# Kernel optimization log

Hardware: AMD Instinct MI355X
Metric: run time of the kernel (lower is better)

The kernel has to match this reference:

```python
import jax, jax.numpy as jnp
import numpy as np

NUM_HEADS = 8
EPS_OT = 0.05    # self.eps
BETA_T = 1.0     # self.beta_t
N_ITERS = 100    # Sinkhorn max_iter (reference runs all iterations; torch breaks early on convergence)


def setup_inputs() -> dict:
    key = jax.random.key(0)
    ks = jax.random.split(key, 10)
    B, N1, N2 = 16, 256, 576
    dim_t, dim_v, dim_out = 512, 512, 512
    s = 0.02  # conv1d k=1 init scale (stand-in for torch default init)
    f32 = jnp.float32
    return {
        "F_t": jax.random.normal(ks[0], (B, N1, dim_t), f32),
        "F_s": jax.random.normal(ks[1], (B, N2, dim_v), f32),
        # Conv1d(kernel_size=1) weights, squeezed to [out, in]; biases default-on in nn.Conv1d
        "Wq": jax.random.normal(ks[2], (dim_out, dim_t), f32) * s,
        "bq": jnp.zeros((dim_out,), f32),
        "Wk": jax.random.normal(ks[3], (dim_out, dim_v), f32) * s,
        "bk": jnp.zeros((dim_out,), f32),
        "Wv": jax.random.normal(ks[4], (dim_out, dim_v), f32) * s,
        "bv": jnp.zeros((dim_out,), f32),
        "Wp": jax.random.normal(ks[5], (dim_out, dim_out), f32) * s,
        "bp": jnp.zeros((dim_out,), f32),
    }


def sinkhorn_log_exp_sum(C, log_mu, log_nu, eps):
    # C: [BH, N1, N2]; fixed-length log-domain Sinkhorn.
    BH, N1, N2 = C.shape
    u0 = jnp.zeros((BH, N1), C.dtype)
    v0 = jnp.zeros((BH, N2), C.dtype)

    def body(carry, _):
        u, v = carry
        # single K per iteration; both u and v updates use the OLD (u, v), matching torch code
        K = (-C + u[:, :, None] + v[:, None, :]) / eps
        u_new = eps * (log_mu - jax.scipy.special.logsumexp(K, axis=2)) + u
        v_new = eps * (log_nu - jax.scipy.special.logsumexp(K, axis=1)) + v
        return (u_new, v_new), None

    (u, v), _ = jax.lax.scan(jax.checkpoint(body), (u0, v0), None, length=N_ITERS)
    return jnp.exp((-C + u[:, :, None] + v[:, None, :]) / eps)


def _l2norm(x, eps=1e-12):
    return x / jnp.maximum(jnp.linalg.norm(x, axis=-1, keepdims=True), eps)


def reference(F_t, F_s, Wq, bq, Wk, bk, Wv, bv, Wp, bp):
    B, N1, _ = F_t.shape
    N2 = F_s.shape[1]
    H = NUM_HEADS
    dim_out = Wq.shape[0]
    hd = dim_out // H

    # Conv1d(kernel=1) == pointwise linear over channel dim
    q = (F_t @ Wq.T + bq).reshape(B, N1, H, hd)
    k = (F_s @ Wk.T + bk).reshape(B, N2, H, hd)
    v = (F_s @ Wv.T + bv).reshape(B, N2, H, hd)

    q = _l2norm(q)
    k = _l2norm(k)

    sim = jnp.einsum('bnkc,bmkc->bknm', q, k) * BETA_T  # [B,H,N1,N2]
    wdist = (1.0 - sim).reshape(B * H, N1, N2)
    sim_f = sim.reshape(B * H, N1, N2)

    log_mu = jnp.log(jnp.asarray(1.0 / N1 + 1e-8, sim.dtype))
    log_nu = jnp.log(jnp.asarray(1.0 / N2 + 1e-8, sim.dtype))
    T = sinkhorn_log_exp_sum(wdist, log_mu, log_nu, EPS_OT)

    score_map = (N1 * N2 * sim_f * T).reshape(B, H, N1, N2)  # attn_drop = identity (p=0)
    F_t_a = jnp.einsum('bknm,bmkc->bnkc', score_map, v).reshape(B, N1, dim_out)
    F_t_a = F_t_a @ Wp.T + bp
    # torch: F_t_a / F_t_a.norm(dim=-1, keepdim=True)  (plain division, no eps clamp)
    F_t_a = F_t_a / jnp.linalg.norm(F_t_a, axis=-1, keepdims=True)
    return F_t_a  # proj_drop = identity (p=0)
```

## Files before the change

### kernel.cpp

```cpp
#include <hip/hip_runtime.h>
#include <math.h>

#define EPS_OT 0.05f
#define INV_EPS 20.0f

typedef unsigned short ushort_t;
typedef __attribute__((ext_vector_type(8))) short short8;
typedef __attribute__((ext_vector_type(4))) float f32x4;
union Pk { uint4 u; short8 s; };

__device__ __forceinline__ unsigned int f2bf(float f) {
  unsigned int u = __float_as_uint(f);
  return (u + 0x7FFFu + ((u >> 16) & 1u)) >> 16;
}
__device__ __forceinline__ float bf2f(unsigned int u) { return __uint_as_float(u << 16); }

__global__ __launch_bounds__(256) void pack_k(const float* __restrict__ F_t,
                                              const float* __restrict__ F_s,
                                              const float* __restrict__ Wq,
                                              const float* __restrict__ Wk,
                                              const float* __restrict__ Wv,
                                              const float* __restrict__ Wp,
                                              ushort_t* __restrict__ Fth, ushort_t* __restrict__ Ftl,
                                              ushort_t* __restrict__ Fsh, ushort_t* __restrict__ Fsl,
                                              ushort_t* __restrict__ Wqh, ushort_t* __restrict__ Wql,
                                              ushort_t* __restrict__ Wkh, ushort_t* __restrict__ Wkl,
                                              ushort_t* __restrict__ Wvh, ushort_t* __restrict__ Wvl,
                                              ushort_t* __restrict__ Wph) {
  const int blk = blockIdx.x;
  const float* src; ushort_t* dh; ushort_t* dl; size_t off;
  if (blk < 2048)      { src = F_t; dh = Fth; dl = Ftl; off = (size_t)blk * 1024; }
  else if (blk < 6656) { src = F_s; dh = Fsh; dl = Fsl; off = (size_t)(blk - 2048) * 1024; }
  else if (blk < 6912) { src = Wq;  dh = Wqh; dl = Wql; off = (size_t)(blk - 6656) * 1024; }
  else if (blk < 7168) { src = Wk;  dh = Wkh; dl = Wkl; off = (size_t)(blk - 6912) * 1024; }
  else if (blk < 7424) { src = Wv;  dh = Wvh; dl = Wvl; off = (size_t)(blk - 7168) * 1024; }
  else                 { src = Wp;  dh = Wph; dl = nullptr; off = (size_t)(blk - 7424) * 1024; }
  const size_t i = off + (size_t)threadIdx.x * 4;
  float4 f = *(const float4*)(src + i);
  unsigned int h0 = f2bf(f.x), h1 = f2bf(f.y), h2 = f2bf(f.z), h3 = f2bf(f.w);
  uint2 hh; hh.x = h0 | (h1 << 16); hh.y = h2 | (h3 << 16);
  *(uint2*)(dh + i) = hh;
  if (dl) {
    uint2 ll;
    ll.x = f2bf(f.x - bf2f(h0)) | (f2bf(f.y - bf2f(h1)) << 16);
    ll.y = f2bf(f.z - bf2f(h2)) | (f2bf(f.w - bf2f(h3)) << 16);
    *(uint2*)(dl + i) = ll;
  }
}

#define GEMM_HL_BODY()                                                                      \
  f32x4 acc[4] = {};                                                                        \
  for (int k0 = 0; k0 < 512; k0 += 64) {                                                    \
    uint4 a0 = *(const uint4*)(Xp_h + k0), a1 = *(const uint4*)(Xp_h + k0 + 8);             \
    uint4 b0 = *(const uint4*)(Xp_l + k0), b1 = *(const uint4*)(Xp_l + k0 + 8);             \
    uint4 c0 = *(const uint4*)(Wp_h + k0), c1 = *(const uint4*)(Wp_h + k0 + 8);             \
    uint4 d0 = *(const uint4*)(Wp_l + k0), d1 = *(const uint4*)(Wp_l + k0 + 8);             \
    __syncthreads();                                                                        \
    *(uint4*)&Xh[r][cg * 16] = a0; *(uint4*)&Xh[r][cg * 16 + 8] = a1;                       \
    *(uint4*)&Xl[r][cg * 16] = b0; *(uint4*)&Xl[r][cg * 16 + 8] = b1;                       \
    *(uint4*)&Wh[r][cg * 16] = c0; *(uint4*)&Wh[r][cg * 16 + 8] = c1;                       \
    *(uint4*)&Wl[r][cg * 16] = d0; *(uint4*)&Wl[r][cg * 16 + 8] = d1;                       \
    __syncthreads();                                                                        \
    _Pragma("unroll") for (int kst = 0; kst < 2; ++kst) {                                   \
      short8 ah = *(const short8*)&Xh[16 * w + li][kst * 32 + 8 * lg];                      \
      short8 al = *(const short8*)&Xl[16 * w + li][kst * 32 + 8 * lg];                      \
      _Pragma("unroll") for (int nt = 0; nt < 4; ++nt) {                                    \
        short8 bh = *(const short8*)&Wh[nt * 16 + li][kst * 32 + 8 * lg];                   \
        short8 bl = *(const short8*)&Wl[nt * 16 + li][kst * 32 + 8 * lg];                   \
        acc[nt] = __builtin_amdgcn_mfma_f32_16x16x32_bf16(ah, bh, acc[nt], 0, 0, 0);        \
        acc[nt] = __builtin_amdgcn_mfma_f32_16x16x32_bf16(ah, bl, acc[nt], 0, 0, 0);        \
        acc[nt] = __builtin_amdgcn_mfma_f32_16x16x32_bf16(al, bh, acc[nt], 0, 0, 0);        \
      }                                                                                     \
    }                                                                                       \
  }

#define GEMM_PL_BODY()                                                                      \
  f32x4 acc[4] = {};                                                                        \
  for (int k0 = 0; k0 < 512; k0 += 64) {                                                    \
    uint4 a0 = *(const uint4*)(Xp_h + k0), a1 = *(const uint4*)(Xp_h + k0 + 8);             \
    uint4 c0 = *(const uint4*)(Wp_h + k0), c1 = *(const uint4*)(Wp_h + k0 + 8);             \
    __syncthreads();                                                                        \
    *(uint4*)&Xh[r][cg * 16] = a0; *(uint4*)&Xh[r][cg * 16 + 8] = a1;                       \
    *(uint4*)&Wh[r][cg * 16] = c0; *(uint4*)&Wh[r][cg * 16 + 8] = c1;                       \
    __syncthreads();                                                                        \
    _Pragma("unroll") for (int kst = 0; kst < 2; ++kst) {                                   \
      short8 ah = *(const short8*)&Xh[16 * w + li][kst * 32 + 8 * lg];                      \
      _Pragma("unroll") for (int nt = 0; nt < 4; ++nt) {                                    \
        short8 bh = *(const short8*)&Wh[nt * 16 + li][kst * 32 + 8 * lg];                   \
        acc[nt] = __builtin_amdgcn_mfma_f32_16x16x32_bf16(ah, bh, acc[nt], 0, 0, 0);        \
      }                                                                                     \
    }                                                                                       \
  }

__global__ __launch_bounds__(256) void gemmnorm2_k(const ushort_t* __restrict__ Xg_h,
                                                   const ushort_t* __restrict__ Xg_l,
                                                   const ushort_t* __restrict__ Wg_h,
                                                   const ushort_t* __restrict__ Wg_l,
                                                   const float* __restrict__ bias,
                                                   ushort_t* __restrict__ oh,
                                                   ushort_t* __restrict__ ol, int Nn) {
  __shared__ ushort_t Xh[64][72], Xl[64][72], Wh[64][72], Wl[64][72];
  const int tid = threadIdx.x;
  const int w = tid >> 6, l = tid & 63, li = l & 15, lg = l >> 4;
  const int r = tid >> 2, cg = tid & 3;
  const int m0 = blockIdx.x << 6;
  const int h = blockIdx.y, n0 = h << 6;
  const ushort_t* Xp_h = Xg_h + (size_t)(m0 + r) * 512 + cg * 16;
  const ushort_t* Xp_l = Xg_l + (size_t)(m0 + r) * 512 + cg * 16;
  const ushort_t* Wp_h = Wg_h + (size_t)(n0 + r) * 512 + cg * 16;
  const ushort_t* Wp_l = Wg_l + (size_t)(n0 + r) * 512 + cg * 16;
  GEMM_HL_BODY()
  float v[4][4];
  float ss[4] = {0.f, 0.f, 0.f, 0.f};
#pragma unroll
  for (int nt = 0; nt < 4; ++nt) {
    float bb = bias[n0 + nt * 16 + li];
#pragma unroll
    for (int reg = 0; reg < 4; ++reg) {
      float y = acc[nt][reg] + bb;
      v[nt][reg] = y;
      ss[reg] = fmaf(y, y, ss[reg]);
    }
  }
#pragma unroll
  for (int off = 1; off < 16; off <<= 1)
#pragma unroll
    for (int reg = 0; reg < 4; ++reg) ss[reg] += __shfl_xor(ss[reg], off, 64);
  const int b = m0 / Nn;
  const int nbase = m0 - b * Nn;
  const size_t base = ((size_t)(b * 8 + h) * Nn + nbase + 16 * w + 4 * lg) * 64;
#pragma unroll
  for (int reg = 0; reg < 4; ++reg) {
    float inv = 1.0f / fmaxf(sqrtf(ss[reg]), 1e-12f);
#pragma unroll
    for (int nt = 0; nt < 4; ++nt) {
      float y = v[nt][reg] * inv;
      unsigned int hi = f2bf(y);
      size_t idx = base + (size_t)reg * 64 + nt * 16 + li;
      oh[idx] = (ushort_t)hi;
      ol[idx] = (ushort_t)f2bf(y - bf2f(hi));
    }
  }
}

__global__ __launch_bounds__(256) void gemmtrans2_k(const ushort_t* __restrict__ Xg_h,
                                                    const ushort_t* __restrict__ Wg_h,
                                                    const float* __restrict__ bias,
                                                    ushort_t* __restrict__ vt) {
  __shared__ ushort_t Xh[64][72], Wh[64][72];
  __shared__ ushort_t Vs[64 * 73];
  const int tid = threadIdx.x;
  const int w = tid >> 6, l = tid & 63, li = l & 15, lg = l >> 4;
  const int r = tid >> 2, cg = tid & 3;
  const int m0 = blockIdx.x << 6;
  const int h = blockIdx.y, n0 = h << 6;
  const ushort_t* Xp_h = Xg_h + (size_t)(m0 + r) * 512 + cg * 16;
  const ushort_t* Wp_h = Wg_h + (size_t)(n0 + r) * 512 + cg * 16;
  GEMM_PL_BODY()
#pragma unroll
  for (int nt = 0; nt < 4; ++nt) {
    float bb = bias[n0 + nt * 16 + li];
#pragma unroll
    for (int reg = 0; reg < 4; ++reg)
      Vs[(16 * w + 4 * lg + reg) * 73 + nt * 16 + li] = (ushort_t)f2bf(acc[nt][reg] + bb);
  }
  __syncthreads();
  const int a9 = m0 >> 6;
  const int b = a9 / 9;
  const int nbase = m0 - b * 576;
  const int s = b * 8 + h;
  const int c = tid >> 2, q4 = tid & 3;
  ushort_t tmp[16];
#pragma unroll
  for (int jj = 0; jj < 16; ++jj) tmp[jj] = Vs[(q4 * 16 + jj) * 73 + c];
  ushort_t* op = vt + ((size_t)s * 64 + c) * 576 + nbase + q4 * 16;
  *(uint4*)op = *(uint4*)&tmp[0];
  *(uint4*)(op + 8) = *(uint4*)&tmp[8];
}

__global__ __launch_bounds__(256) void gemmplain_k(const ushort_t* __restrict__ Xg_h,
                                                   const ushort_t* __restrict__ Wg_h,
                                                   const float* __restrict__ bias,
                                                   float* __restrict__ Y) {
  __shared__ ushort_t Xh[64][72], Wh[64][72];
  const int tid = threadIdx.x;
  const int w = tid >> 6, l = tid & 63, li = l & 15, lg = l >> 4;
  const int r = tid >> 2, cg = tid & 3;
  const int m0 = blockIdx.x << 6, n0 = blockIdx.y << 6;
  const ushort_t* Xp_h = Xg_h + (size_t)(m0 + r) * 512 + cg * 16;
  const ushort_t* Wp_h = Wg_h + (size_t)(n0 + r) * 512 + cg * 16;
  GEMM_PL_BODY()
#pragma unroll
  for (int nt = 0; nt < 4; ++nt) {
    float bb = bias[n0 + nt * 16 + li];
#pragma unroll
    for (int reg = 0; reg < 4; ++reg)
      Y[(size_t)(m0 + 16 * w + 4 * lg + reg) * 512 + n0 + nt * 16 + li] = acc[nt][reg] + bb;
  }
}

__global__ __launch_bounds__(256) void simE2_k(const ushort_t* __restrict__ qh,
                                               const ushort_t* __restrict__ ql,
                                               const ushort_t* __restrict__ kh,
                                               const ushort_t* __restrict__ kl,
                                               ushort_t* __restrict__ E) {
  const int s = blockIdx.x, i0 = blockIdx.y << 6, j0 = blockIdx.z << 6;
  const int tid = threadIdx.x;
  const int w = tid >> 6, l = tid & 63, li = l & 15, lg = l >> 4;
  const size_t qoff = ((size_t)s * 256 + i0 + 16 * w + li) * 64 + 8 * lg;
  short8 aH0 = *(const short8*)(qh + qoff), aH1 = *(const short8*)(qh + qoff + 32);
  short8 aL0 = *(const short8*)(ql + qoff), aL1 = *(const short8*)(ql + qoff + 32);
  f32x4 acc[4] = {};
#pragma unroll
  for (int nt = 0; nt < 4; ++nt) {
    const size_t koff = ((size_t)s * 576 + j0 + nt * 16 + li) * 64 + 8 * lg;
    short8 bH0 = *(const short8*)(kh + koff), bH1 = *(const short8*)(kh + koff + 32);
    short8 bL0 = *(const short8*)(kl + koff), bL1 = *(const short8*)(kl + koff + 32);
    acc[nt] = __builtin_amdgcn_mfma_f32_16x16x32_bf16(aH0, bH0, acc[nt], 0, 0, 0);
    acc[nt] = __builtin_amdgcn_mfma_f32_16x16x32_bf16(aH1, bH1, acc[nt], 0, 0, 0);
    acc[nt] = __builtin_amdgcn_mfma_f32_16x16x32_bf16(aH0, bL0, acc[nt], 0, 0, 0);
    acc[nt] = __builtin_amdgcn_mfma_f32_16x16x32_bf16(aH1, bL1, acc[nt], 0, 0, 0);
    acc[nt] = __builtin_amdgcn_mfma_f32_16x16x32_bf16(aL0, bH0, acc[nt], 0, 0, 0);
    acc[nt] = __builtin_amdgcn_mfma_f32_16x16x32_bf16(aL1, bH1, acc[nt], 0, 0, 0);
  }
  ushort_t* Ep = E + (size_t)s * 147456;
#pragma unroll
  for (int nt = 0; nt < 4; ++nt)
#pragma unroll
    for (int reg = 0; reg < 4; ++reg) {
      float e = __expf((acc[nt][reg] - 1.0f) * INV_EPS);
      Ep[(size_t)(i0 + 16 * w + 4 * lg + reg) * 576 + j0 + nt * 16 + li] = (ushort_t)f2bf(e);
    }
}

#define SK_SMEM 147456

__global__ __launch_bounds__(1024, 1) void sinkhorn8_k(const ushort_t* __restrict__ E,
                                                       float* __restrict__ gA,
                                                       float* __restrict__ gB,
                                                       unsigned long long* __restrict__ gpart,
                                                       float C_mu, float C_nu) {
  extern __shared__ char smem[];
  const int g = blockIdx.x, s = g >> 1, rh = g & 1, pg = g ^ 1;
  const int tid = threadIdx.x, w = tid >> 6, l = tid & 63, li = l & 15, lg = l >> 4;
  unsigned long long* myP = gpart + (size_t)g * 1152;
  const unsigned long long* prP = gpart + (size_t)pg * 1152;

  ushort_t* Elds = (ushort_t*)smem;
  {
    const uint4* Eg = (const uint4*)(E + (size_t)s * 147456 + (size_t)rh * 73728);
    uint4* El4 = (uint4*)Elds;
    for (int idx = tid; idx < 9216; idx += 1024) El4[idx] = Eg[idx];
  }
  __syncthreads();

  short8 afr[9];
#pragma unroll
  for (int rt = 0; rt < 8; ++rt)
    afr[rt] = *(const short8*)(Elds + (rt * 16 + li) * 576 + w * 32 + 8 * lg);
  const int rtx = w & 7, ktx = 16 + (w >> 3);
  afr[8] = *(const short8*)(Elds + (rtx * 16 + li) * 576 + ktx * 32 + 8 * lg);
  const int ktB = w >> 2, ntb = (w & 3) * 9;
  short8 bfr[9];
#pragma unroll
  for (int p9 = 0; p9 < 9; ++p9) {
    const ushort_t* p = Elds + (ktB * 32 + 8 * lg) * 576 + (ntb + p9) * 16 + li;
    Pk pk;
    pk.u.x = (unsigned int)p[0]    | ((unsigned int)p[576]  << 16);
    pk.u.y = (unsigned int)p[1152] | ((unsigned int)p[1728] << 16);
    pk.u.z = (unsigned int)p[2304] | ((unsigned int)p[2880] << 16);
    pk.u.w = (unsigned int)p[3456] | ((unsigned int)p[4032] << 16);
    bfr[p9] = pk.s;
  }
  __syncthreads();

  float* uu = (float*)smem;
  float* vv = uu + 128;
  ushort_t* au = (ushort_t*)(vv + 576);
  ushort_t* bv = au + 128;
  float* rpart = (float*)(au + 384 + 320);
  float* colp = rpart + 2304;
  float* cso = colp + 2304;

  if (tid < 128) { uu[tid] = 0.0f; au[tid] = (ushort_t)0x3F80; }
  if (tid < 576) { vv[tid] = 0.0f; bv[tid] = (ushort_t)0x3F80; }
  __syncthreads();

  for (int t = 0; t < 100; ++t) {
    {
      Pk ah; ah.u = *(const uint4*)(au + ktB * 32 + 8 * lg);
      float* cp = colp + (w >> 2) * 576;
#pragma unroll
      for (int p9 = 0; p9 < 9; ++p9) {
        f32x4 a2 = {0.f, 0.f, 0.f, 0.f};
        a2 = __builtin_amdgcn_mfma_f32_16x16x32_bf16(ah.s, bfr[p9], a2, 0, 0, 0);
        if (l < 16) cp[(ntb + p9) * 16 + l] = a2[0];
      }
    }
    __syncthreads();
    const int par = t & 1;
    if (tid < 576) {
      float cs = colp[tid] + colp[576 + tid] + colp[1152 + tid] + colp[1728 + tid];
      cso[tid] = cs;
      unsigned long long pv = (unsigned long long)__float_as_uint(cs) |
                              ((unsigned long long)(unsigned int)(t + 1) << 32);
      __hip_atomic_store(&myP[par * 576 + tid], pv, __ATOMIC_RELAXED, __HIP_MEMORY_SCOPE_AGENT);
    }
    {
      Pk bh, bhx;
      bh.u = *(const uint4*)(bv + w * 32 + 8 * lg);
      bhx.u = *(const uint4*)(bv + ktx * 32 + 8 * lg);
#pragma unroll
      for (int rt = 0; rt < 8; ++rt) {
        f32x4 a1 = {0.f, 0.f, 0.f, 0.f};
        a1 = __builtin_amdgcn_mfma_f32_16x16x32_bf16(bh.s, afr[rt], a1, 0, 0, 0);
        if (l < 16) rpart[w * 128 + rt * 16 + l] = a1[0];
      }
      f32x4 a1 = {0.f, 0.f, 0.f, 0.f};
      a1 = __builtin_amdgcn_mfma_f32_16x16x32_bf16(bhx.s, afr[8], a1, 0, 0, 0);
      if (l < 16) rpart[ktx * 128 + rtx * 16 + l] = a1[0];
    }
    __syncthreads();
    if (tid < 128) {
      float rs = 0.0f;
#pragma unroll
      for (int kc = 0; kc < 18; ++kc) rs += rpart[kc * 128 + tid];
      float un = C_mu - EPS_OT * __logf(rs);
      uu[tid] = un;
      au[tid] = (ushort_t)f2bf(__expf(fminf(fmaxf(un * INV_EPS, -80.f), 80.f)));
    } else if (tid < 704) {
      const int j = tid - 128;
      const unsigned int tg = (unsigned int)(t + 1);
      unsigned long long p0;
      for (;;) {
        p0 = __hip_atomic_load(&prP[par * 576 + j], __ATOMIC_RELAXED, __HIP_MEMORY_SCOPE_AGENT);
        if ((unsigned int)(p0 >> 32) == tg) break;
        __builtin_amdgcn_s_sleep(1);
      }
      float tot = cso[j] + __uint_as_float((unsigned int)p0);
      float vn = C_nu - EPS_OT * __logf(tot);
      vv[j] = vn;
      bv[j] = (ushort_t)f2bf(__expf(fminf(fmaxf(vn * INV_EPS, -80.f), 80.f)));
    }
    __syncthreads();
  }
  if (tid < 128) gA[(size_t)s * 256 + rh * 128 + tid] = uu[tid] * INV_EPS;
  if (rh == 0 && tid < 576) gB[(size_t)s * 576 + tid] = vv[tid] * INV_EPS + 11.9012851f;
}

__global__ __launch_bounds__(256) void scorev2_k(const ushort_t* __restrict__ E,
                                                 const ushort_t* __restrict__ vt,
                                                 const float* __restrict__ gA,
                                                 const float* __restrict__ gB,
                                                 ushort_t* __restrict__ Y) {
  __shared__ float gBs[576];
  const int s = blockIdx.x, i0 = blockIdx.y << 6;
  const int tid = threadIdx.x;
  const int w = tid >> 6, l = tid & 63, li = l & 15, lg = l >> 4;
  for (int j = tid; j < 576; j += 256) gBs[j] = gB[(size_t)s * 576 + j];
  const float ga = gA[(size_t)s * 256 + i0 + 16 * w + li];
  const ushort_t* Erow = E + (size_t)s * 147456 + (size_t)(i0 + 16 * w + li) * 576;
  f32x4 acc[4] = {};
  __syncthreads();
  for (int kst = 0; kst < 18; ++kst) {
    const int jb = kst * 32 + 8 * lg;
    Pk eu; eu.u = *(const uint4*)(Erow + jb);
    float pv[8];
#pragma unroll
    for (int jj = 0; jj < 8; ++jj) {
      unsigned int us = (unsigned int)(unsigned short)eu.s[jj];
      float e = bf2f(us);
      float le = __logf(e);
      pv[jj] = (1.0f + EPS_OT * le) * __expf(le + ga + gBs[jb + jj]);
    }
    Pk ph, pl;
#pragma unroll
    for (int jj = 0; jj < 8; ++jj) {
      unsigned int h = f2bf(pv[jj]);
      ((unsigned short*)&ph.s)[jj] = (unsigned short)h;
      ((unsigned short*)&pl.s)[jj] = (unsigned short)f2bf(pv[jj] - bf2f(h));
    }
#pragma unroll
    for (int nt = 0; nt < 4; ++nt) {
      Pk vf; vf.u = *(const uint4*)(vt + ((size_t)s * 64 + nt * 16 + li) * 576 + jb);
      acc[nt] = __builtin_amdgcn_mfma_f32_16x16x32_bf16(ph.s, vf.s, acc[nt], 0, 0, 0);
      acc[nt] = __builtin_amdgcn_mfma_f32_16x16x32_bf16(pl.s, vf.s, acc[nt], 0, 0, 0);
    }
  }
  const int b = s >> 3, h = s & 7;
#pragma unroll
  for (int nt = 0; nt < 4; ++nt)
#pragma unroll
    for (int reg = 0; reg < 4; ++reg)
      Y[((size_t)(b * 256 + i0 + 16 * w + 4 * lg + reg) << 9) + (h << 6) + nt * 16 + li] =
          (ushort_t)f2bf(acc[nt][reg]);
}

__global__ __launch_bounds__(256) void rownorm_k(const float* __restrict__ X,
                                                 float* __restrict__ out) {
  const size_t row = blockIdx.x;
  const int tid = threadIdx.x;
  float x0 = X[(row << 9) + tid], x1 = X[(row << 9) + 256 + tid];
  float st = fmaf(x0, x0, x1 * x1);
#pragma unroll
  for (int off = 32; off; off >>= 1) st += __shfl_xor(st, off, 64);
  __shared__ float ps[4];
  if ((tid & 63) == 0) ps[tid >> 6] = st;
  __syncthreads();
  const float inv = 1.0f / sqrtf(ps[0] + ps[1] + ps[2] + ps[3]);
  out[(row << 9) + tid] = x0 * inv;
  out[(row << 9) + 256 + tid] = x1 * inv;
}

extern "C" void kernel_launch(void* const* d_in, const int* in_sizes, int n_in,
                              void* d_out, int out_size, void* d_ws, size_t ws_size,
                              hipStream_t stream) {
  const float* F_t = (const float*)d_in[0];
  const float* F_s = (const float*)d_in[1];
  const float* Wq = (const float*)d_in[2];
  const float* bq = (const float*)d_in[3];
  const float* Wk = (const float*)d_in[4];
  const float* bk = (const float*)d_in[5];
  const float* Wv = (const float*)d_in[6];
  const float* bvb = (const float*)d_in[7];
  const float* Wp = (const float*)d_in[8];
  const float* bp = (const float*)d_in[9];
  float* out = (float*)d_out;

  ushort_t* u0 = (ushort_t*)d_ws;
  ushort_t* Fth = u0;
  ushort_t* Ftl = Fth + 2097152;
  ushort_t* Fsh = Ftl + 2097152;
  ushort_t* Fsl = Fsh + 4718592;
  ushort_t* Wqh = Fsl + 4718592;
  ushort_t* Wql = Wqh + 262144;
  ushort_t* Wkh = Wql + 262144;
  ushort_t* Wkl = Wkh + 262144;
  ushort_t* Wvh = Wkl + 262144;
  ushort_t* Wvl = Wvh + 262144;
  ushort_t* Wph = Wvl + 262144;
  ushort_t* qh = Wph + 262144;
  ushort_t* ql = qh + 2097152;
  ushort_t* kh = ql + 2097152;
  ushort_t* kl = kh + 4718592;
  ushort_t* vt = kl + 4718592;
  ushort_t* Eb = vt + 4718592;
  ushort_t* T0b = Eb + 18874368;
  float* T1 = (float*)(T0b + 2097152);
  float* gA = T1 + 2097152;
  float* gB = gA + 32768;
  unsigned long long* gpart = (unsigned long long*)(gB + 73728);

  const float C_mu = (float)(0.05 * log(1.0 / 256.0 + 1e-8));
  const float C_nu = (float)(0.05 * log(1.0 / 576.0 + 1e-8));

  (void)hipFuncSetAttribute((const void*)sinkhorn8_k,
                            hipFuncAttributeMaxDynamicSharedMemorySize, SK_SMEM);

  pack_k<<<7680, 256, 0, stream>>>(F_t, F_s, Wq, Wk, Wv, Wp, Fth, Ftl, Fsh, Fsl,
                                   Wqh, Wql, Wkh, Wkl, Wvh, Wvl, Wph);
  gemmnorm2_k<<<dim3(64, 8), 256, 0, stream>>>(Fth, Ftl, Wqh, Wql, bq, qh, ql, 256);
  gemmnorm2_k<<<dim3(144, 8), 256, 0, stream>>>(Fsh, Fsl, Wkh, Wkl, bk, kh, kl, 576);
  gemmtrans2_k<<<dim3(144, 8), 256, 0, stream>>>(Fsh, Wvh, bvb, vt);
  simE2_k<<<dim3(128, 4, 9), 256, 0, stream>>>(qh, ql, kh, kl, Eb);
  sinkhorn8_k<<<256, 1024, SK_SMEM, stream>>>(Eb, gA, gB, gpart, C_mu, C_nu);
  scorev2_k<<<dim3(128, 4), 256, 0, stream>>>(Eb, vt, gA, gB, T0b);
  gemmplain_k<<<dim3(64, 8), 256, 0, stream>>>(T0b, Wph, bp, T1);
  rownorm_k<<<4096, 256, 0, stream>>>(T1, out);
}
```

Measured before the change: 385.7 us.

## Defer cross-block v update into next iteration to overlap partner polling

The Sinkhorn kernel now waits on the partner block's column partial sums at the start of the next iteration, after issuing that iteration's column MFMAs, rather than at the end of the current one. The final v update moves to a tail step after the loop. This hides the inter-block spin-wait latency behind independent MFMA work. The row-sum reduction is also spread over 512 threads using shuffles instead of 128 threads doing serial sums. The cost is more complex iteration ordering, which needs care so the column MFMAs read the correct u/v state.

```diff
diff --git a/kernel.cpp b/kernel.cpp
--- a/kernel.cpp
+++ b/kernel.cpp
@@ -235,7 +235,7 @@
 
 #define SK_SMEM 147456
 
-__global__ __launch_bounds__(1024, 1) void sinkhorn8_k(const ushort_t* __restrict__ E,
+__global__ __launch_bounds__(1024, 1) void sinkhorn9_k(const ushort_t* __restrict__ E,
                                                        float* __restrict__ gA,
                                                        float* __restrict__ gB,
                                                        unsigned long long* __restrict__ gpart,
@@ -286,10 +286,19 @@
   if (tid < 576) { vv[tid] = 0.0f; bv[tid] = (ushort_t)0x3F80; }
   __syncthreads();
 
+  const int jj = tid - 128;
+  const bool poller = (tid >= 128) && (tid < 704);
+
   for (int t = 0; t < 100; ++t) {
+    const int par = t & 1;
+    unsigned long long p0 = 0;
+    if (poller && t > 0)
+      p0 = __hip_atomic_load(&prP[(par ^ 1) * 576 + jj], __ATOMIC_RELAXED,
+                             __HIP_MEMORY_SCOPE_AGENT);
+    __builtin_amdgcn_sched_barrier(0);
     {
       Pk ah; ah.u = *(const uint4*)(au + ktB * 32 + 8 * lg);
-      float* cp = colp + (w >> 2) * 576;
+      float* cp = colp + ktB * 576;
 #pragma unroll
       for (int p9 = 0; p9 < 9; ++p9) {
         f32x4 a2 = {0.f, 0.f, 0.f, 0.f};
@@ -297,8 +306,19 @@
         if (l < 16) cp[(ntb + p9) * 16 + l] = a2[0];
       }
     }
+    if (poller && t > 0) {
+      const unsigned int tg = (unsigned int)t;
+      while ((unsigned int)(p0 >> 32) != tg) {
+        __builtin_amdgcn_s_sleep(1);
+        p0 = __hip_atomic_load(&prP[(par ^ 1) * 576 + jj], __ATOMIC_RELAXED,
+                               __HIP_MEMORY_SCOPE_AGENT);
+      }
+      float tot = cso[jj] + __uint_as_float((unsigned int)p0);
+      float vn = C_nu - EPS_OT * __logf(tot);
+      vv[jj] = vn;
+      bv[jj] = (ushort_t)f2bf(__expf(fminf(fmaxf(vn * INV_EPS, -80.f), 80.f)));
+    }
     __syncthreads();
-    const int par = t & 1;
     if (tid < 576) {
       float cs = colp[tid] + colp[576 + tid] + colp[1152 + tid] + colp[1728 + tid];
       cso[tid] = cs;
@@ -321,29 +341,32 @@
       if (l < 16) rpart[ktx * 128 + rtx * 16 + l] = a1[0];
     }
     __syncthreads();
-    if (tid < 128) {
-      float rs = 0.0f;
-#pragma unroll
-      for (int kc = 0; kc < 18; ++kc) rs += rpart[kc * 128 + tid];
-      float un = C_mu - EPS_OT * __logf(rs);
-      uu[tid] = un;
-      au[tid] = (ushort_t)f2bf(__expf(fminf(fmaxf(un * INV_EPS, -80.f), 80.f)));
-    } else if (tid < 704) {
-      const int j = tid - 128;
-      const unsigned int tg = (unsigned int)(t + 1);
-      unsigned long long p0;
-      for (;;) {
-        p0 = __hip_atomic_load(&prP[par * 576 + j], __ATOMIC_RELAXED, __HIP_MEMORY_SCOPE_AGENT);
-        if ((unsigned int)(p0 >> 32) == tg) break;
-        __builtin_amdgcn_s_sleep(1);
+    if (tid < 512) {
+      const int r = tid >> 2, q = tid & 3;
+      float rs = rpart[q * 128 + r] + rpart[(q + 4) * 128 + r] +
+                 rpart[(q + 8) * 128 + r] + rpart[(q + 12) * 128 + r];
+      if (q < 2) rs += rpart[(16 + q) * 128 + r];
+      rs += __shfl_xor(rs, 1, 64);
+      rs += __shfl_xor(rs, 2, 64);
+      if (q == 0) {
+        float un = C_mu - EPS_OT * __logf(rs);
+        uu[r] = un;
+        au[r] = (ushort_t)f2bf(__expf(fminf(fmaxf(un * INV_EPS, -80.f), 80.f)));
       }
-      float tot = cso[j] + __uint_as_float((unsigned int)p0);
-      float vn = C_nu - EPS_OT * __logf(tot);
-      vv[j] = vn;
-      bv[j] = (ushort_t)f2bf(__expf(fminf(fmaxf(vn * INV_EPS, -80.f), 80.f)));
     }
     __syncthreads();
   }
+  if (rh == 0 && poller) {
+    unsigned long long p0;
+    for (;;) {
+      p0 = __hip_atomic_load(&prP[576 + jj], __ATOMIC_RELAXED, __HIP_MEMORY_SCOPE_AGENT);
+      if ((unsigned int)(p0 >> 32) == 100u) break;
+      __builtin_amdgcn_s_sleep(1);
+    }
+    float tot = cso[jj] + __uint_as_float((unsigned int)p0);
+    vv[jj] = C_nu - EPS_OT * __logf(tot);
+  }
+  __syncthreads();
   if (tid < 128) gA[(size_t)s * 256 + rh * 128 + tid] = uu[tid] * INV_EPS;
   if (rh == 0 && tid < 576) gB[(size_t)s * 576 + tid] = vv[tid] * INV_EPS + 11.9012851f;
 }
@@ -454,7 +477,7 @@
   const float C_mu = (float)(0.05 * log(1.0 / 256.0 + 1e-8));
   const float C_nu = (float)(0.05 * log(1.0 / 576.0 + 1e-8));
 
-  (void)hipFuncSetAttribute((const void*)sinkhorn8_k,
+  (void)hipFuncSetAttribute((const void*)sinkhorn9_k,
                             hipFuncAttributeMaxDynamicSharedMemorySize, SK_SMEM);
 
   pack_k<<<7680, 256, 0, stream>>>(F_t, F_s, Wq, Wk, Wv, Wp, Fth, Ftl, Fsh, Fsl,
@@ -463,7 +486,7 @@
   gemmnorm2_k<<<dim3(144, 8), 256, 0, stream>>>(Fsh, Fsl, Wkh, Wkl, bk, kh, kl, 576);
   gemmtrans2_k<<<dim3(144, 8), 256, 0, stream>>>(Fsh, Wvh, bvb, vt);
   simE2_k<<<dim3(128, 4, 9), 256, 0, stream>>>(qh, ql, kh, kl, Eb);
-  sinkhorn8_k<<<256, 1024, SK_SMEM, stream>>>(Eb, gA, gB, gpart, C_mu, C_nu);
+  sinkhorn9_k<<<256, 1024, SK_SMEM, stream>>>(Eb, gA, gB, gpart, C_mu, C_nu);
   scorev2_k<<<dim3(128, 4), 256, 0, stream>>>(Eb, vt, gA, gB, T0b);
   gemmplain_k<<<dim3(64, 8), 256, 0, stream>>>(T0b, Wph, bp, T1);
   rownorm_k<<<4096, 256, 0, stream>>>(T1, out);
```

Result: slower. 410.1 us (+6.3%).
